# Optimization experiments

Hardware: AMD Instinct MI355X
Metric: run time of the kernel (lower is better)

Reference implementation:

```python
import jax, jax.numpy as jnp
import numpy as np

POOL_K = 8        # predictor_kernel_size
THRESH = 0.05     # predictor_threshold
EPS = 1e-5        # masked_fill value


def _round_ste(x):
    # straight-through round (forward: round)
    return x + jax.lax.stop_gradient(jnp.round(x) - x)


def _quant_act_uint(x, scale, bits):
    # Brevitas Uint8ActPerTensorFloat-style fake quant: unsigned, per-tensor scale
    n = 2.0 ** bits - 1.0
    return jnp.clip(_round_ste(x / scale), 0.0, n) * scale


def _quant_weight_per_oc(w, bits):
    # signed, narrow-range, per-output-channel scaling: s = max|w| / (2^(b-1)-1)
    n = 2.0 ** (bits - 1) - 1.0
    s = jnp.max(jnp.abs(w), axis=(1, 2, 3), keepdims=True) / n
    return jnp.clip(_round_ste(w / s), -n, n) * s


def _conv(x, w):
    return jax.lax.conv_general_dilated(
        x, w, window_strides=(1, 1), padding=((1, 1), (1, 1)),
        dimension_numbers=('NCHW', 'OIHW', 'NCHW'))


def _predictor_mask(x):
    # AvgPool2d(8) (stride=kernel) -> threshold -> nearest upsample back to HxW
    B, C, H, W = x.shape
    pooled = x.reshape(B, C, H // POOL_K, POOL_K, W // POOL_K, POOL_K).mean(axis=(3, 5))
    m = pooled >= THRESH
    m = jnp.repeat(jnp.repeat(m, POOL_K, axis=2), POOL_K, axis=3)  # nearest interp
    return jax.lax.stop_gradient(m)  # mask.detach()


def setup_inputs() -> dict:
    key = jax.random.key(0)
    k1, k2, k3 = jax.random.split(key, 3)
    x = jax.random.normal(k1, (32, 128, 56, 56), jnp.float32)
    w_high = jax.random.normal(k2, (128, 128, 3, 3), jnp.float32) * 0.05
    w_low = jax.random.normal(k3, (128, 128, 3, 3), jnp.float32) * 0.05
    return {
        'x': x,
        'w_high': w_high,
        'w_low': w_low,
        'act_scale_high': jnp.float32(0.02),
        'act_scale_low': jnp.float32(0.04),
    }


def reference(x, w_high, w_low, act_scale_high, act_scale_low):
    mask = _predictor_mask(x)                 # [B,C,H,W] bool
    x_high = jnp.where(mask, x, EPS)          # masked_fill(~mask, 1e-5)
    x_low = jnp.where(mask, EPS, x)           # masked_fill(mask, 1e-5)
    y_high = _conv(_quant_act_uint(x_high, act_scale_high, 8),
                   _quant_weight_per_oc(w_high, 8))
    y_low = _conv(_quant_act_uint(x_low, act_scale_low, 4),
                  _quant_weight_per_oc(w_low, 4))
    return y_high + y_low
```

## Files before the change

### kernel.cpp

```cpp
#include <hip/hip_runtime.h>
#include <hip/hip_bf16.h>
#include <stdint.h>

#define BATCH 32
#define CH 128
#define HH 56
#define WW 56
#define HW 3136
#define M_TOTAL (BATCH*HW)
#define PLANE ((size_t)M_TOTAL * 16)

using int4v   = __attribute__((ext_vector_type(4))) int;
using float4v = __attribute__((ext_vector_type(4))) float;

#define WQB_OFF 0
#define SCB_OFF 294912
#define ZP_OFF  296448
#define AQN_OFF 296704

#define GLD_LDS16(g, l)                                                        \
  __builtin_amdgcn_global_load_lds(                                            \
      (const __attribute__((address_space(1))) void*)(g),                      \
      (__attribute__((address_space(3))) void*)(l), 16, 0, 0)

__global__ __launch_bounds__(256) void quant_w_kernel(
    const float* __restrict__ wh, const float* __restrict__ wl,
    const float* __restrict__ p_sh, const float* __restrict__ p_sl,
    char* __restrict__ wqb, float* __restrict__ scb, int* __restrict__ zp) {
  int blk = blockIdx.x;
  int which = blk >> 7, oc = blk & 127;
  if (blk == 0 && threadIdx.x < 64)
    zp[threadIdx.x] = (threadIdx.x < 32) ? 0x80808080 : 0;
  const float* src = (which ? wl : wh) + (size_t)oc * 1152;
  float n = which ? 7.0f : 127.0f;

  __shared__ float red[256];
  __shared__ int ired[256];
  float m = 0.0f;
  for (int e = threadIdx.x; e < 1152; e += 256) m = fmaxf(m, fabsf(src[e]));
  red[threadIdx.x] = m;
  __syncthreads();
  for (int s = 128; s > 0; s >>= 1) {
    if (threadIdx.x < s) red[threadIdx.x] = fmaxf(red[threadIdx.x], red[threadIdx.x + s]);
    __syncthreads();
  }
  float scale = red[0] / n;

  int partial = 0;
  for (int e = threadIdx.x; e < 1152; e += 256) {
    int tt = e >> 7, ic = e & 127;
    float q = rintf(src[ic * 9 + tt] / scale);
    q = fminf(fmaxf(q, -n), n);
    int k = (int)q;
    partial += k;
    wqb[((size_t)tt * 128 + oc) * 256 + which * 128 + ic] = (char)k;
  }
  ired[threadIdx.x] = partial;
  __syncthreads();
  for (int s = 128; s > 0; s >>= 1) {
    if (threadIdx.x < s) ired[threadIdx.x] += ired[threadIdx.x + s];
    __syncthreads();
  }
  if (threadIdx.x == 0) {
    float s_act = which ? p_sl[0] : p_sh[0];
    float sc = s_act * scale;
    if (which == 0) {
      scb[oc] = sc;
      scb[256 + oc] = sc * 128.0f * (float)ired[0];
    } else {
      scb[128 + oc] = sc;
    }
  }
}

#define KSTR 484
__global__ __launch_bounds__(256) void maskquant_kernel(
    const float* __restrict__ x, const float* __restrict__ p_sh,
    const float* __restrict__ p_sl, char* __restrict__ aqn) {
  int bi = blockIdx.x;
  int cg = bi & 7;
  int bb = bi >> 3;
  int b = bb / 7, band = bb - b * 7;
  __shared__ float sx[16 * KSTR];
  __shared__ float smk[16 * 7];
  int t = threadIdx.x;
  #pragma unroll
  for (int i = 0; i < 7; ++i) {
    int idx = i * 256 + t;
    int k = idx / 112, rem = idx - k * 112;
    int r = rem / 14, w4 = rem - r * 14;
    *(float4v*)(sx + k * KSTR + r * 60 + w4 * 4) =
        *(const float4v*)(x + ((size_t)(b * 128 + cg * 16 + k)) * HW
                            + (band * 8 + r) * 56 + w4 * 4);
  }
  __syncthreads();
  if (t < 112) {
    int k = t / 7, bw = t - (t / 7) * 7;
    float s = 0.0f;
    #pragma unroll
    for (int r = 0; r < 8; ++r)
      #pragma unroll
      for (int j = 0; j < 8; ++j)
        s += sx[k * KSTR + r * 60 + bw * 8 + j];
    smk[t] = (s * (1.0f / 64.0f) >= 0.05f) ? 1.0f : 0.0f;
  }
  __syncthreads();
  float shs = p_sh[0], sls = p_sl[0];
  #pragma unroll
  for (int it = 0; it < 2; ++it) {
    int pos = it * 256 + t;
    if (pos < 448) {
      int r = pos / 56, w = pos - r * 56;
      int h = band * 8 + r;
      size_t gp = (size_t)b * HW + (size_t)h * 56 + w;
      int hw_[4] = {0, 0, 0, 0}, lw_[4] = {0, 0, 0, 0};
      int mcell = w >> 3;
      #pragma unroll
      for (int k = 0; k < 16; ++k) {
        float xv = sx[k * KSTR + r * 60 + w];
        bool mk = smk[k * 7 + mcell] != 0.0f;
        float xh = mk ? xv : 1e-5f;
        int kh = (int)fminf(fmaxf(rintf(xh / shs), 0.0f), 255.0f) - 128;
        float xl = mk ? 1e-5f : xv;
        int kl = (int)fminf(fmaxf(rintf(xl / sls), 0.0f), 15.0f);
        hw_[k >> 2] |= (kh & 0xff) << ((k & 3) * 8);
        lw_[k >> 2] |= (kl & 0xff) << ((k & 3) * 8);
      }
      *(int4v*)(aqn + ((size_t)cg * M_TOTAL + gp) * 16) =
          (int4v){hw_[0], hw_[1], hw_[2], hw_[3]};
      *(int4v*)(aqn + ((size_t)(8 + cg) * M_TOTAL + gp) * 16) =
          (int4v){lw_[0], lw_[1], lw_[2], lw_[3]};
    }
  }
}

__global__ __launch_bounds__(256, 4) void conv_mfma_kernel(
    const char* __restrict__ wqb,
    const char* __restrict__ aqn,
    const char* __restrict__ zp,
    const float* __restrict__ scb,
    float* __restrict__ out) {
  __shared__ __align__(16) char As[160 * 64];
  __shared__ __align__(16) char Bs[192 * 64];

  int tid = threadIdx.x;
  int lane = tid & 63, wv = tid >> 6;
  int wm = wv >> 1, wn = wv & 1;
  int lr = lane & 15, quad = lane >> 4;
  int bx = blockIdx.x;
  int m0 = (((bx & 7) * 98) + (bx >> 3)) * 128;
  int oc0 = blockIdx.y * 64;

  int ng = (wv < 2) ? 3 : 2;
  int sgrp[3] = {wv, wv + 4, wv + 8};
  const char* abase[3];
  const char* zbase[3];
  int avalid[3], ah[3];
  #pragma unroll
  for (int j = 0; j < 3; ++j) {
    int slot = sgrp[j] * 16 + (lane >> 2);
    int q = ((lane & 3) ^ (slot >> 1)) & 3;
    int p = m0 + slot - 16;
    int pv = (p >= 0) && (p < M_TOTAL);
    int pc = pv ? p : 0;
    int bb = pc / HW, rem = pc - bb * HW;
    int hh = rem / 56;
    abase[j] = aqn + (size_t)q * PLANE + (size_t)pc * 16;
    zbase[j] = zp + q * 16;
    avalid[j] = pv;
    ah[j] = hh;
  }
  const char* bbase[3];
  #pragma unroll
  for (int i = 0; i < 3; ++i) {
    int slot = wv * 48 + i * 16 + (lane >> 2);
    int qp = (((lane & 3) ^ (slot >> 1)) & 3) * 16;
    int dwi_s = slot >> 6, ocr = slot & 63;
    bbase[i] = wqb + ((size_t)(dwi_s * 128 + oc0 + ocr)) * 256 + qp;
  }
  int lo_ok[4], hi_ok[4];
  #pragma unroll
  for (int mi = 0; mi < 4; ++mi) {
    int m = m0 + wm * 64 + mi * 16 + lr;
    int w = (m % HW) % 56;
    lo_ok[mi] = (w > 0);
    hi_ok[mi] = (w < 55);
  }

  int4v acch[4][2], accl[4][2];
  #pragma unroll
  for (int mi = 0; mi < 4; ++mi)
    #pragma unroll
    for (int ni = 0; ni < 2; ++ni) {
      acch[mi][ni] = (int4v){0, 0, 0, 0};
      accl[mi][ni] = (int4v){0, 0, 0, 0};
    }

  for (int dh3 = 0; dh3 < 3; ++dh3) {
    int dh = dh3 - 1;
    const char* asrc[3];
    size_t astr[3];
    #pragma unroll
    for (int j = 0; j < 3; ++j) {
      int h2 = ah[j] + dh;
      bool ok = avalid[j] && ((unsigned)h2 < (unsigned)HH);
      asrc[j] = ok ? (abase[j] + dh * (56 * 16)) : zbase[j];
      astr[j] = ok ? (size_t)4 * PLANE : (size_t)64;
    }
    const size_t boff = (size_t)dh3 * 98304;
    #pragma unroll
    for (int icc = 0; icc < 4; ++icc) {
      int ic0 = icc * 64;
      const bool high = (icc < 2);
      const int patv = high ? (int)0x80808080 : 0;
      const int4v pat = (int4v){patv, patv, patv, patv};
      __syncthreads();
      #pragma unroll
      for (int j = 0; j < 3; ++j)
        if (j < ng) GLD_LDS16(asrc[j] + icc * astr[j], As + sgrp[j] * 1024);
      #pragma unroll
      for (int i = 0; i < 3; ++i)
        GLD_LDS16(bbase[i] + boff + ic0, Bs + (wv * 48 + i * 16) * 64);
      __syncthreads();

      #pragma unroll
      for (int dwi = 0; dwi < 3; ++dwi) {
        int4v af[4], bf[2];
        #pragma unroll
        for (int mi = 0; mi < 4; ++mi) {
          int sA = wm * 64 + mi * 16 + lr + 15 + dwi;
          af[mi] = *(const int4v*)(As + sA * 64 + (((quad ^ (sA >> 1)) & 3) * 16));
          bool ok = (dwi == 1) | (dwi == 0 ? lo_ok[mi] : hi_ok[mi]);
          af[mi] = ok ? af[mi] : pat;
        }
        #pragma unroll
        for (int ni = 0; ni < 2; ++ni) {
          int sB = dwi * 64 + wn * 32 + ni * 16 + lr;
          bf[ni] = *(const int4v*)(Bs + sB * 64 + (((quad ^ (sB >> 1)) & 3) * 16));
        }
        if (high) {
          #pragma unroll
          for (int mi = 0; mi < 4; ++mi)
            #pragma unroll
            for (int ni = 0; ni < 2; ++ni)
              acch[mi][ni] = __builtin_amdgcn_mfma_i32_16x16x64_i8(
                  af[mi], bf[ni], acch[mi][ni], 0, 0, 0);
        } else {
          #pragma unroll
          for (int mi = 0; mi < 4; ++mi)
            #pragma unroll
            for (int ni = 0; ni < 2; ++ni)
              accl[mi][ni] = __builtin_amdgcn_mfma_i32_16x16x64_i8(
                  af[mi], bf[ni], accl[mi][ni], 0, 0, 0);
        }
      }
    }
  }

  #pragma unroll
  for (int mi = 0; mi < 4; ++mi) {
    int m = m0 + wm * 64 + mi * 16 + quad * 4;
    int b = m / HW, r = m - b * HW;
    float* obase = out + (size_t)b * (CH * HW) + r;
    #pragma unroll
    for (int ni = 0; ni < 2; ++ni) {
      int oc = oc0 + wn * 32 + ni * 16 + lr;
      float sch = scb[oc], scl = scb[128 + oc], bs = scb[256 + oc];
      float4v f;
      #pragma unroll
      for (int rg = 0; rg < 4; ++rg)
        f[rg] = sch * (float)acch[mi][ni][rg] + scl * (float)accl[mi][ni][rg] + bs;
      *(float4v*)(obase + (size_t)oc * HW) = f;
    }
  }
}

extern "C" void kernel_launch(void* const* d_in, const int* in_sizes, int n_in,
                              void* d_out, int out_size, void* d_ws, size_t ws_size,
                              hipStream_t stream) {
  const float* x  = (const float*)d_in[0];
  const float* wh = (const float*)d_in[1];
  const float* wl = (const float*)d_in[2];
  const float* sh = (const float*)d_in[3];
  const float* sl = (const float*)d_in[4];
  float* out = (float*)d_out;

  char* ws = (char*)d_ws;
  char* wqb  = ws + WQB_OFF;
  float* scb = (float*)(ws + SCB_OFF);
  int* zp    = (int*)(ws + ZP_OFF);
  char* aqn  = ws + AQN_OFF;

  quant_w_kernel<<<dim3(256), dim3(256), 0, stream>>>(wh, wl, sh, sl, wqb, scb, zp);
  maskquant_kernel<<<dim3(BATCH * 7 * 8), dim3(256), 0, stream>>>(x, sh, sl, aqn);
  conv_mfma_kernel<<<dim3(M_TOTAL / 128, 2), dim3(256), 0, stream>>>(
      wqb, aqn, (const char*)zp, scb, out);
}
```

Before: 185.5 us.

## Double-buffer conv LDS stages, merge prep kernels, add nontemporal stores and setprio

```diff
diff --git a/kernel.cpp b/kernel.cpp
--- a/kernel.cpp
+++ b/kernel.cpp
@@ -23,67 +23,71 @@
       (const __attribute__((address_space(1))) void*)(g),                      \
       (__attribute__((address_space(3))) void*)(l), 16, 0, 0)
 
-__global__ __launch_bounds__(256) void quant_w_kernel(
+#define KSTR 484
+
+__global__ __launch_bounds__(256) void prep_kernel(
+    const float* __restrict__ x,
     const float* __restrict__ wh, const float* __restrict__ wl,
     const float* __restrict__ p_sh, const float* __restrict__ p_sl,
-    char* __restrict__ wqb, float* __restrict__ scb, int* __restrict__ zp) {
-  int blk = blockIdx.x;
-  int which = blk >> 7, oc = blk & 127;
-  if (blk == 0 && threadIdx.x < 64)
-    zp[threadIdx.x] = (threadIdx.x < 32) ? 0x80808080 : 0;
-  const float* src = (which ? wl : wh) + (size_t)oc * 1152;
-  float n = which ? 7.0f : 127.0f;
-
-  __shared__ float red[256];
-  __shared__ int ired[256];
-  float m = 0.0f;
-  for (int e = threadIdx.x; e < 1152; e += 256) m = fmaxf(m, fabsf(src[e]));
-  red[threadIdx.x] = m;
-  __syncthreads();
-  for (int s = 128; s > 0; s >>= 1) {
-    if (threadIdx.x < s) red[threadIdx.x] = fmaxf(red[threadIdx.x], red[threadIdx.x + s]);
+    char* __restrict__ wqb, float* __restrict__ scb, int* __restrict__ zp,
+    char* __restrict__ aqn) {
+  __shared__ __align__(16) float smem[16 * KSTR + 128];
+  int t = threadIdx.x;
+
+  if (blockIdx.x >= BATCH * 7 * 8) {
+    int blk = blockIdx.x - BATCH * 7 * 8;
+    int which = blk >> 7, oc = blk & 127;
+    if (blk == 0 && t < 64)
+      zp[t] = (t < 32) ? 0x80808080 : 0;
+    const float* src = (which ? wl : wh) + (size_t)oc * 1152;
+    float n = which ? 7.0f : 127.0f;
+    float* red = smem;
+    int* ired = (int*)(smem + 256);
+
+    float m = 0.0f;
+    for (int e = t; e < 1152; e += 256) m = fmaxf(m, fabsf(src[e]));
+    red[t] = m;
     __syncthreads();
-  }
-  float scale = red[0] / n;
-
-  int partial = 0;
-  for (int e = threadIdx.x; e < 1152; e += 256) {
-    int tt = e >> 7, ic = e & 127;
-    float q = rintf(src[ic * 9 + tt] / scale);
-    q = fminf(fmaxf(q, -n), n);
-    int k = (int)q;
-    partial += k;
-    wqb[((size_t)tt * 128 + oc) * 256 + which * 128 + ic] = (char)k;
-  }
-  ired[threadIdx.x] = partial;
-  __syncthreads();
-  for (int s = 128; s > 0; s >>= 1) {
-    if (threadIdx.x < s) ired[threadIdx.x] += ired[threadIdx.x + s];
+    for (int s = 128; s > 0; s >>= 1) {
+      if (t < s) red[t] = fmaxf(red[t], red[t + s]);
+      __syncthreads();
+    }
+    float scale = red[0] / n;
+
+    int partial = 0;
+    for (int e = t; e < 1152; e += 256) {
+      int tt = e >> 7, ic = e & 127;
+      float q = rintf(src[ic * 9 + tt] / scale);
+      q = fminf(fmaxf(q, -n), n);
+      int k = (int)q;
+      partial += k;
+      wqb[((size_t)tt * 128 + oc) * 256 + which * 128 + ic] = (char)k;
+    }
+    ired[t] = partial;
     __syncthreads();
-  }
-  if (threadIdx.x == 0) {
-    float s_act = which ? p_sl[0] : p_sh[0];
-    float sc = s_act * scale;
-    if (which == 0) {
-      scb[oc] = sc;
-      scb[256 + oc] = sc * 128.0f * (float)ired[0];
-    } else {
-      scb[128 + oc] = sc;
-    }
-  }
-}
-
-#define KSTR 484
-__global__ __launch_bounds__(256) void maskquant_kernel(
-    const float* __restrict__ x, const float* __restrict__ p_sh,
-    const float* __restrict__ p_sl, char* __restrict__ aqn) {
+    for (int s = 128; s > 0; s >>= 1) {
+      if (t < s) ired[t] += ired[t + s];
+      __syncthreads();
+    }
+    if (t == 0) {
+      float s_act = which ? p_sl[0] : p_sh[0];
+      float sc = s_act * scale;
+      if (which == 0) {
+        scb[oc] = sc;
+        scb[256 + oc] = sc * 128.0f * (float)ired[0];
+      } else {
+        scb[128 + oc] = sc;
+      }
+    }
+    return;
+  }
+
   int bi = blockIdx.x;
   int cg = bi & 7;
   int bb = bi >> 3;
   int b = bb / 7, band = bb - b * 7;
-  __shared__ float sx[16 * KSTR];
-  __shared__ float smk[16 * 7];
-  int t = threadIdx.x;
+  float* sx = smem;
+  float* smk = smem + 16 * KSTR;
   #pragma unroll
   for (int i = 0; i < 7; ++i) {
     int idx = i * 256 + t;
@@ -134,14 +138,14 @@
   }
 }
 
-__global__ __launch_bounds__(256, 4) void conv_mfma_kernel(
+__global__ __launch_bounds__(256, 3) void conv_mfma_kernel(
     const char* __restrict__ wqb,
     const char* __restrict__ aqn,
     const char* __restrict__ zp,
     const float* __restrict__ scb,
     float* __restrict__ out) {
-  __shared__ __align__(16) char As[160 * 64];
-  __shared__ __align__(16) char Bs[192 * 64];
+  __shared__ __align__(16) char As[2][160 * 64];
+  __shared__ __align__(16) char Bs[2][192 * 64];
 
   int tid = threadIdx.x;
   int lane = tid & 63, wv = tid >> 6;
@@ -196,65 +200,72 @@
       accl[mi][ni] = (int4v){0, 0, 0, 0};
     }
 
-  for (int dh3 = 0; dh3 < 3; ++dh3) {
+  auto stage = [&](int s, char* A, char* B) {
+    int dh3 = s >> 2, icc = s & 3;
     int dh = dh3 - 1;
-    const char* asrc[3];
-    size_t astr[3];
     #pragma unroll
     for (int j = 0; j < 3; ++j) {
-      int h2 = ah[j] + dh;
-      bool ok = avalid[j] && ((unsigned)h2 < (unsigned)HH);
-      asrc[j] = ok ? (abase[j] + dh * (56 * 16)) : zbase[j];
-      astr[j] = ok ? (size_t)4 * PLANE : (size_t)64;
-    }
-    const size_t boff = (size_t)dh3 * 98304;
-    #pragma unroll
-    for (int icc = 0; icc < 4; ++icc) {
-      int ic0 = icc * 64;
-      const bool high = (icc < 2);
-      const int patv = high ? (int)0x80808080 : 0;
-      const int4v pat = (int4v){patv, patv, patv, patv};
-      __syncthreads();
-      #pragma unroll
-      for (int j = 0; j < 3; ++j)
-        if (j < ng) GLD_LDS16(asrc[j] + icc * astr[j], As + sgrp[j] * 1024);
-      #pragma unroll
-      for (int i = 0; i < 3; ++i)
-        GLD_LDS16(bbase[i] + boff + ic0, Bs + (wv * 48 + i * 16) * 64);
-      __syncthreads();
-
-      #pragma unroll
-      for (int dwi = 0; dwi < 3; ++dwi) {
-        int4v af[4], bf[2];
+      if (j < ng) {
+        int h2 = ah[j] + dh;
+        bool ok = avalid[j] && ((unsigned)h2 < (unsigned)HH);
+        const char* p = ok ? (abase[j] + dh * (56 * 16) + (size_t)icc * (4 * PLANE))
+                           : (zbase[j] + icc * 64);
+        GLD_LDS16(p, A + sgrp[j] * 1024);
+      }
+    }
+    #pragma unroll
+    for (int i = 0; i < 3; ++i)
+      GLD_LDS16(bbase[i] + (size_t)dh3 * 98304 + icc * 64,
+                B + (wv * 48 + i * 16) * 64);
+  };
+
+  auto compute = [&](int s, const char* A, const char* B) {
+    int icc = s & 3;
+    const bool high = (icc < 2);
+    const int patv = high ? (int)0x80808080 : 0;
+    const int4v pat = (int4v){patv, patv, patv, patv};
+    #pragma unroll
+    for (int dwi = 0; dwi < 3; ++dwi) {
+      int4v af[4], bf[2];
+      #pragma unroll
+      for (int mi = 0; mi < 4; ++mi) {
+        int sA = wm * 64 + mi * 16 + lr + 15 + dwi;
+        af[mi] = *(const int4v*)(A + sA * 64 + (((quad ^ (sA >> 1)) & 3) * 16));
+        bool ok = (dwi == 1) | (dwi == 0 ? lo_ok[mi] : hi_ok[mi]);
+        af[mi] = ok ? af[mi] : pat;
+      }
+      #pragma unroll
+      for (int ni = 0; ni < 2; ++ni) {
+        int sB = dwi * 64 + wn * 32 + ni * 16 + lr;
+        bf[ni] = *(const int4v*)(B + sB * 64 + (((quad ^ (sB >> 1)) & 3) * 16));
+      }
+      __builtin_amdgcn_s_setprio(1);
+      if (high) {
         #pragma unroll
-        for (int mi = 0; mi < 4; ++mi) {
-          int sA = wm * 64 + mi * 16 + lr + 15 + dwi;
-          af[mi] = *(const int4v*)(As + sA * 64 + (((quad ^ (sA >> 1)) & 3) * 16));
-          bool ok = (dwi == 1) | (dwi == 0 ? lo_ok[mi] : hi_ok[mi]);
-          af[mi] = ok ? af[mi] : pat;
-        }
+        for (int mi = 0; mi < 4; ++mi)
+          #pragma unroll
+          for (int ni = 0; ni < 2; ++ni)
+            acch[mi][ni] = __builtin_amdgcn_mfma_i32_16x16x64_i8(
+                af[mi], bf[ni], acch[mi][ni], 0, 0, 0);
+      } else {
         #pragma unroll
-        for (int ni = 0; ni < 2; ++ni) {
-          int sB = dwi * 64 + wn * 32 + ni * 16 + lr;
-          bf[ni] = *(const int4v*)(Bs + sB * 64 + (((quad ^ (sB >> 1)) & 3) * 16));
-        }
-        if (high) {
+        for (int mi = 0; mi < 4; ++mi)
           #pragma unroll
-          for (int mi = 0; mi < 4; ++mi)
-            #pragma unroll
-            for (int ni = 0; ni < 2; ++ni)
-              acch[mi][ni] = __builtin_amdgcn_mfma_i32_16x16x64_i8(
-                  af[mi], bf[ni], acch[mi][ni], 0, 0, 0);
-        } else {
-          #pragma unroll
-          for (int mi = 0; mi < 4; ++mi)
-            #pragma unroll
-            for (int ni = 0; ni < 2; ++ni)
-              accl[mi][ni] = __builtin_amdgcn_mfma_i32_16x16x64_i8(
-                  af[mi], bf[ni], accl[mi][ni], 0, 0, 0);
-        }
-      }
-    }
+          for (int ni = 0; ni < 2; ++ni)
+            accl[mi][ni] = __builtin_amdgcn_mfma_i32_16x16x64_i8(
+                af[mi], bf[ni], accl[mi][ni], 0, 0, 0);
+      }
+      __builtin_amdgcn_s_setprio(0);
+    }
+  };
+
+  stage(0, As[0], Bs[0]);
+  __syncthreads();
+  #pragma unroll
+  for (int s = 0; s < 12; ++s) {
+    if (s < 11) stage(s + 1, As[(s + 1) & 1], Bs[(s + 1) & 1]);
+    compute(s, As[s & 1], Bs[s & 1]);
+    __syncthreads();
   }
 
   #pragma unroll
@@ -270,7 +281,7 @@
       #pragma unroll
       for (int rg = 0; rg < 4; ++rg)
         f[rg] = sch * (float)acch[mi][ni][rg] + scl * (float)accl[mi][ni][rg] + bs;
-      *(float4v*)(obase + (size_t)oc * HW) = f;
+      __builtin_nontemporal_store(f, (float4v*)(obase + (size_t)oc * HW));
     }
   }
 }
@@ -291,8 +302,8 @@
   int* zp    = (int*)(ws + ZP_OFF);
   char* aqn  = ws + AQN_OFF;
 
-  quant_w_kernel<<<dim3(256), dim3(256), 0, stream>>>(wh, wl, sh, sl, wqb, scb, zp);
-  maskquant_kernel<<<dim3(BATCH * 7 * 8), dim3(256), 0, stream>>>(x, sh, sl, aqn);
+  prep_kernel<<<dim3(BATCH * 7 * 8 + 256), dim3(256), 0, stream>>>(
+      x, wh, wl, sh, sl, wqb, scb, zp, aqn);
   conv_mfma_kernel<<<dim3(M_TOTAL / 128, 2), dim3(256), 0, stream>>>(
       wqb, aqn, (const char*)zp, scb, out);
 }
```

Result: faster. 157.7 us (-15.0%).
